# Kernel optimization log

Hardware: AMD Instinct MI355X
Metric: run time of the kernel (lower is better)

## Reference

```python
import jax, jax.numpy as jnp
import numpy as np

N_NODES = 50000
N_EDGES = 800000
D_FEAT = 128
D_EDGE = 64
N_HEADS = 4
OUT_DIM = 32
HID = N_HEADS * OUT_DIM  # 128


def segment_softmax(logits, seg, num_segments):
    # jraph.segment_softmax: subtract per-segment max, exp, normalize by per-segment sum
    seg_max = jax.ops.segment_max(logits, seg, num_segments=num_segments)
    e = jnp.exp(logits - seg_max[seg])
    denom = jax.ops.segment_sum(e, seg, num_segments=num_segments)
    return e / denom[seg]


def setup_inputs() -> dict:
    key = jax.random.key(0)
    ks = jax.random.split(key, 12)
    s = 1.0 / np.sqrt(D_FEAT)
    se = 1.0 / np.sqrt(D_EDGE)
    return {
        "nodes": jax.random.normal(ks[0], (N_NODES, D_FEAT), jnp.float32),
        "edges": jax.random.normal(ks[1], (N_EDGES, D_EDGE), jnp.float32),
        "senders": jax.random.randint(ks[2], (N_EDGES,), 0, N_NODES, jnp.int32),
        "receivers": jax.random.randint(ks[3], (N_EDGES,), 0, N_NODES, jnp.int32),
        "Wq": jax.random.normal(ks[4], (D_FEAT, HID), jnp.float32) * s,
        "bq": jnp.zeros((HID,), jnp.float32),
        "Wk": jax.random.normal(ks[5], (D_FEAT, HID), jnp.float32) * s,
        "bk": jnp.zeros((HID,), jnp.float32),
        "Wv": jax.random.normal(ks[6], (D_FEAT, HID), jnp.float32) * s,
        "bv": jnp.zeros((HID,), jnp.float32),
        "We": jax.random.normal(ks[7], (D_EDGE, HID), jnp.float32) * se,
        "Wu": jax.random.normal(ks[8], (D_FEAT, OUT_DIM), jnp.float32) * s,
        "bu": jnp.zeros((OUT_DIM,), jnp.float32),
    }


def reference(nodes, edges, senders, receivers, Wq, bq, Wk, bk, Wv, bv, We, Wu, bu):
    n_nodes = nodes.shape[0]
    send_feats = nodes[senders]    # [E, D]
    recv_feats = nodes[receivers]  # [E, D]

    q = (recv_feats @ Wq + bq).reshape(-1, N_HEADS, OUT_DIM)
    k = (send_feats @ Wk + bk).reshape(-1, N_HEADS, OUT_DIM)
    v = (send_feats @ Wv + bv).reshape(-1, N_HEADS, OUT_DIM)
    e = (edges @ We).reshape(-1, N_HEADS, OUT_DIM)

    attn = (q * k).sum(-1) / jnp.sqrt(jnp.asarray(OUT_DIM, q.dtype))  # [E, H]
    attn = segment_softmax(attn, receivers, n_nodes)                  # [E, H]

    msgs = (attn[:, :, None] * (v + e)).mean(axis=1)                  # [E, OUT_DIM]
    aggr = jax.ops.segment_sum(msgs, receivers, num_segments=n_nodes) # [N, OUT_DIM]

    feats = nodes @ Wu + bu
    return jax.nn.relu(feats + aggr)
```

## Files before the change

### kernel.cpp

```cpp
#include <hip/hip_runtime.h>
#include <math.h>

#define N_NODES 50000
#define N_EDGES 800000
#define D_FEAT 128
#define D_EDGE 64
#define HID 128
#define OUT_DIM 32

typedef unsigned short u16;
typedef short bf16x8 __attribute__((ext_vector_type(8)));
typedef float f32x4 __attribute__((ext_vector_type(4)));

__device__ __forceinline__ u16 f2bf(float x) {
    unsigned u = __float_as_uint(x);
    unsigned r = (u >> 16) & 1u;
    return (u16)((u + 0x7FFFu + r) >> 16);
}
__device__ __forceinline__ float bf2f(u16 s) { return __uint_as_float(((unsigned)s) << 16); }
__device__ __forceinline__ float bflo(unsigned u) { return __uint_as_float(u << 16); }
__device__ __forceinline__ float bfhi(unsigned u) { return __uint_as_float(u & 0xFFFF0000u); }

__global__ void zero_i32(int* __restrict__ p, int n) {
    int i = blockIdx.x * 256 + threadIdx.x;
    if (i < n) p[i] = 0;
}

__global__ void prep_weights(const float* __restrict__ Wq, const float* __restrict__ Wk,
                             const float* __restrict__ Wv, const float* __restrict__ We,
                             const float* __restrict__ Wu,
                             u16* __restrict__ WT_all, u16* __restrict__ WeTg) {
    int id = blockIdx.x * 256 + threadIdx.x;
    if (id < 49152) {
        int m = id >> 14, rem = id & 16383;
        int c = rem >> 7, k = rem & 127;
        const float* W = (m == 0) ? Wq : (m == 1) ? Wk : Wv;
        WT_all[id] = f2bf(W[k * HID + c]);
    } else if (id < 57344) {
        int j = id - 49152;
        int c = j >> 6, k = j & 63;
        WeTg[j] = f2bf(We[k * HID + c]);
    } else {
        int j = id - 57344;
        int c = j >> 7, k = j & 127;
        WT_all[49152 + j] = f2bf(Wu[k * OUT_DIM + c]);
    }
}

__global__ __launch_bounds__(256) void node_qkv_v3(
    const float* __restrict__ nodes, const u16* __restrict__ WT_all,
    const float* __restrict__ bq, const float* __restrict__ bk, const float* __restrict__ bv,
    const float* __restrict__ bu,
    u16* __restrict__ Q, u16* __restrict__ Kk, u16* __restrict__ Vp,
    float* __restrict__ baseout)
{
    __shared__ __align__(16) u16 Alds[4][32 * 136];

    const int tid = threadIdx.x;
    const int wave = tid >> 6, lane = tid & 63;
    const int quad = lane >> 4, l15 = lane & 15;
    const int rowbase = blockIdx.x * 128 + wave * 32;

    u16* As = &Alds[wave][0];
    #pragma unroll
    for (int it = 0; it < 16; ++it) {
        int idx = lane + it * 64;
        int row = idx >> 5, k4 = (idx & 31) * 4;
        float4 v = make_float4(0.f, 0.f, 0.f, 0.f);
        if (rowbase + row < N_NODES)
            v = *(const float4*)&nodes[(size_t)(rowbase + row) * D_FEAT + k4];
        ushort4 b;
        b.x = f2bf(v.x); b.y = f2bf(v.y); b.z = f2bf(v.z); b.w = f2bf(v.w);
        *(ushort4*)&As[row * 136 + k4] = b;
    }

    bf16x8 afr[2][4];
    #pragma unroll
    for (int rt = 0; rt < 2; ++rt)
        #pragma unroll
        for (int ks = 0; ks < 4; ++ks)
            afr[rt][ks] = *(const bf16x8*)&As[(rt * 16 + l15) * 136 + ks * 32 + quad * 8];

    #pragma unroll
    for (int m = 0; m < 3; ++m) {
        const u16* WT = WT_all + (size_t)m * 16384;
        const float* bvec = (m == 0) ? bq : (m == 1) ? bk : bv;
        u16* C = (m == 0) ? Q : (m == 1) ? Kk : Vp;

        f32x4 acc[2][8];
        #pragma unroll
        for (int rt = 0; rt < 2; ++rt)
            #pragma unroll
            for (int ct = 0; ct < 8; ++ct)
                acc[rt][ct] = (f32x4){0.f, 0.f, 0.f, 0.f};

        #pragma unroll
        for (int ks = 0; ks < 4; ++ks) {
            #pragma unroll
            for (int ct = 0; ct < 8; ++ct) {
                bf16x8 b = *(const bf16x8*)&WT[(ct * 16 + l15) * 128 + ks * 32 + quad * 8];
                acc[0][ct] = __builtin_amdgcn_mfma_f32_16x16x32_bf16(afr[0][ks], b, acc[0][ct], 0, 0, 0);
                acc[1][ct] = __builtin_amdgcn_mfma_f32_16x16x32_bf16(afr[1][ks], b, acc[1][ct], 0, 0, 0);
            }
        }

        #pragma unroll
        for (int ct = 0; ct < 8; ++ct) {
            int cbase = ct * 16 + l15;
            float bias = bvec[cbase];
            int oidx = (m == 2) ? ((cbase & 31) * 4 + (cbase >> 5)) : cbase;
            #pragma unroll
            for (int rt = 0; rt < 2; ++rt)
                #pragma unroll
                for (int r = 0; r < 4; ++r) {
                    int n = rowbase + rt * 16 + quad * 4 + r;
                    if (n < N_NODES)
                        C[(size_t)n * HID + oidx] = f2bf(acc[rt][ct][r] + bias);
                }
        }
    }

    {
        const u16* WuT = WT_all + 49152;
        f32x4 accu[2][2];
        #pragma unroll
        for (int rt = 0; rt < 2; ++rt)
            #pragma unroll
            for (int ct = 0; ct < 2; ++ct)
                accu[rt][ct] = (f32x4){0.f, 0.f, 0.f, 0.f};
        #pragma unroll
        for (int ks = 0; ks < 4; ++ks) {
            #pragma unroll
            for (int ct = 0; ct < 2; ++ct) {
                bf16x8 b = *(const bf16x8*)&WuT[(ct * 16 + l15) * 128 + ks * 32 + quad * 8];
                accu[0][ct] = __builtin_amdgcn_mfma_f32_16x16x32_bf16(afr[0][ks], b, accu[0][ct], 0, 0, 0);
                accu[1][ct] = __builtin_amdgcn_mfma_f32_16x16x32_bf16(afr[1][ks], b, accu[1][ct], 0, 0, 0);
            }
        }
        #pragma unroll
        for (int ct = 0; ct < 2; ++ct) {
            int cbase = ct * 16 + l15;
            float bias = bu[cbase];
            #pragma unroll
            for (int rt = 0; rt < 2; ++rt)
                #pragma unroll
                for (int r = 0; r < 4; ++r) {
                    int n = rowbase + rt * 16 + quad * 4 + r;
                    if (n < N_NODES)
                        baseout[(size_t)n * OUT_DIM + cbase] = accu[rt][ct][r] + bias;
                }
        }
    }
}

__global__ void hist_kernel(const int* __restrict__ receivers, int* __restrict__ count) {
    int e = blockIdx.x * 256 + threadIdx.x;
    atomicAdd(&count[receivers[e]], 1);
}

__global__ __launch_bounds__(256) void scan1(const int* __restrict__ count,
                                             int* __restrict__ incl, int* __restrict__ bsum) {
    __shared__ int sh[256];
    int gid = blockIdx.x * 256 + threadIdx.x;
    int v = (gid < N_NODES) ? count[gid] : 0;
    sh[threadIdx.x] = v; __syncthreads();
    #pragma unroll
    for (int off = 1; off < 256; off <<= 1) {
        int t = (threadIdx.x >= off) ? sh[threadIdx.x - off] : 0;
        __syncthreads();
        sh[threadIdx.x] += t;
        __syncthreads();
    }
    if (gid < N_NODES) incl[gid] = sh[threadIdx.x];
    if (threadIdx.x == 255) bsum[blockIdx.x] = sh[255];
}

__global__ __launch_bounds__(256) void scan2(const int* __restrict__ bsum,
                                             int* __restrict__ boff, int nblocks) {
    __shared__ int sh[256];
    int v = (threadIdx.x < nblocks) ? bsum[threadIdx.x] : 0;
    sh[threadIdx.x] = v; __syncthreads();
    #pragma unroll
    for (int off = 1; off < 256; off <<= 1) {
        int t = (threadIdx.x >= off) ? sh[threadIdx.x - off] : 0;
        __syncthreads();
        sh[threadIdx.x] += t;
        __syncthreads();
    }
    boff[threadIdx.x] = sh[threadIdx.x] - v;
}

__global__ __launch_bounds__(256) void scan3(const int* __restrict__ incl,
                                             const int* __restrict__ count,
                                             const int* __restrict__ boff,
                                             int* __restrict__ startp, int* __restrict__ cursor) {
    int gid = blockIdx.x * 256 + threadIdx.x;
    if (gid < N_NODES) {
        int ex = incl[gid] - count[gid] + boff[blockIdx.x];
        startp[gid] = ex;
        cursor[gid] = ex;
    }
    if (gid == 0) startp[N_NODES] = N_EDGES;
}

__global__ void scatter_v3(const int* __restrict__ senders, const int* __restrict__ receivers,
                           int* __restrict__ cursor, int* __restrict__ sorted,
                           int* __restrict__ ssend, int* __restrict__ srecv) {
    int e = blockIdx.x * 256 + threadIdx.x;
    int r = receivers[e];
    int s = senders[e];
    int pos = atomicAdd(&cursor[r], 1);
    sorted[pos] = e;
    ssend[pos] = s;
    srecv[pos] = r;
}

__global__ __launch_bounds__(256) void edge_logits_v3(
    const u16* __restrict__ Q, const u16* __restrict__ K,
    const int* __restrict__ ssend, const int* __restrict__ srecv,
    float* __restrict__ wbuf)
{
    int id = blockIdx.x * 256 + threadIdx.x;
    int i = id >> 1, half = id & 1;
    int s = ssend[i], r = srecv[i];
    const uint4* qp = (const uint4*)&Q[(size_t)r * HID + half * 64];
    const uint4* kp = (const uint4*)&K[(size_t)s * HID + half * 64];
    float a0 = 0.f, a1 = 0.f;
    #pragma unroll
    for (int j = 0; j < 4; ++j) {
        uint4 a = qp[j], b = kp[j];
        a0 += bflo(a.x) * bflo(b.x) + bfhi(a.x) * bfhi(b.x);
        a0 += bflo(a.y) * bflo(b.y) + bfhi(a.y) * bfhi(b.y);
        a0 += bflo(a.z) * bflo(b.z) + bfhi(a.z) * bfhi(b.z);
        a0 += bflo(a.w) * bflo(b.w) + bfhi(a.w) * bfhi(b.w);
    }
    #pragma unroll
    for (int j = 4; j < 8; ++j) {
        uint4 a = qp[j], b = kp[j];
        a1 += bflo(a.x) * bflo(b.x) + bfhi(a.x) * bfhi(b.x);
        a1 += bflo(a.y) * bflo(b.y) + bfhi(a.y) * bfhi(b.y);
        a1 += bflo(a.z) * bflo(b.z) + bfhi(a.z) * bfhi(b.z);
        a1 += bflo(a.w) * bflo(b.w) + bfhi(a.w) * bfhi(b.w);
    }
    const float sc = 0.17677669529663687f;
    float2 o = make_float2(expf(a0 * sc), expf(a1 * sc));
    *(float2*)&wbuf[(size_t)i * 4 + half * 2] = o;
}

__global__ __launch_bounds__(256) void denom_norm3(
    const int* __restrict__ startp, const int* __restrict__ sorted,
    const float* __restrict__ wbuf, float* __restrict__ wnorm)
{
    int id = blockIdx.x * 256 + threadIdx.x;
    int n = id >> 2, j = id & 3;
    if (n >= N_NODES) return;
    int s = startp[n], e = startp[n + 1];
    float4 a = make_float4(0.f, 0.f, 0.f, 0.f);
    for (int i = s + j; i < e; i += 4) {
        float4 w = *(const float4*)&wbuf[(size_t)i * 4];
        a.x += w.x; a.y += w.y; a.z += w.z; a.w += w.w;
    }
    #pragma unroll
    for (int off = 1; off < 4; off <<= 1) {
        a.x += __shfl_xor(a.x, off);
        a.y += __shfl_xor(a.y, off);
        a.z += __shfl_xor(a.z, off);
        a.w += __shfl_xor(a.w, off);
    }
    float4 inv;
    inv.x = 0.25f / a.x; inv.y = 0.25f / a.y; inv.z = 0.25f / a.z; inv.w = 0.25f / a.w;
    for (int i = s + j; i < e; i += 4) {
        float4 w = *(const float4*)&wbuf[(size_t)i * 4];
        w.x *= inv.x; w.y *= inv.y; w.z *= inv.z; w.w *= inv.w;
        *(float4*)&wnorm[(size_t)sorted[i] * 4] = w;
    }
}

__global__ __launch_bounds__(256) void edge_messages_v9(
    const float* __restrict__ edges, const u16* __restrict__ WeTg,
    const u16* __restrict__ Vp, const float* __restrict__ wnorm,
    const int* __restrict__ senders, u16* __restrict__ msg)
{
    __shared__ __align__(16) u16 Ae[4][32 * 72];

    const int tid = threadIdx.x;
    const int wave = tid >> 6, lane = tid & 63;
    const int quad = lane >> 4, l15 = lane & 15;
    const int base = blockIdx.x * 128 + wave * 32;

    int snd8[8];
    float w8[8][4];
    #pragma unroll
    for (int idx = 0; idx < 8; ++idx) {
        int el = base + (idx >> 2) * 16 + quad * 4 + (idx & 3);
        snd8[idx] = senders[el];
        float4 w = *(const float4*)&wnorm[(size_t)el * 4];
        w8[idx][0] = w.x; w8[idx][1] = w.y; w8[idx][2] = w.z; w8[idx][3] = w.w;
    }

    u16* As = &Ae[wave][0];
    #pragma unroll
    for (int it = 0; it < 8; ++it) {
        int idx = lane + it * 64;
        int row = idx >> 4, k4 = (idx & 15) * 4;
        float4 v = *(const float4*)&edges[(size_t)(base + row) * D_EDGE + k4];
        ushort4 b;
        b.x = f2bf(v.x); b.y = f2bf(v.y); b.z = f2bf(v.z); b.w = f2bf(v.w);
        *(ushort4*)&As[row * 72 + k4] = b;
    }

    bf16x8 afr[2][2];
    #pragma unroll
    for (int rt = 0; rt < 2; ++rt)
        #pragma unroll
        for (int ks = 0; ks < 2; ++ks)
            afr[rt][ks] = *(const bf16x8*)&As[(rt * 16 + l15) * 72 + ks * 32 + quad * 8];

    #pragma unroll
    for (int p = 0; p < 2; ++p) {
        const int d = p * 16 + l15;
        ushort4 vp8[8];
        #pragma unroll
        for (int idx = 0; idx < 8; ++idx)
            vp8[idx] = *(const ushort4*)&Vp[(size_t)snd8[idx] * HID + d * 4];

        f32x4 acc[2][4];
        #pragma unroll
        for (int rt = 0; rt < 2; ++rt)
            #pragma unroll
            for (int c = 0; c < 4; ++c)
                acc[rt][c] = (f32x4){0.f, 0.f, 0.f, 0.f};

        #pragma unroll
        for (int ks = 0; ks < 2; ++ks) {
            #pragma unroll
            for (int c = 0; c < 4; ++c) {
                bf16x8 b = *(const bf16x8*)&WeTg[((2 * c + p) * 16 + l15) * 64 + ks * 32 + quad * 8];
                acc[0][c] = __builtin_amdgcn_mfma_f32_16x16x32_bf16(afr[0][ks], b, acc[0][c], 0, 0, 0);
                acc[1][c] = __builtin_amdgcn_mfma_f32_16x16x32_bf16(afr[1][ks], b, acc[1][c], 0, 0, 0);
            }
        }

        #pragma unroll
        for (int idx = 0; idx < 8; ++idx) {
            int rt = idx >> 2, r = idx & 3;
            int el = base + rt * 16 + quad * 4 + r;
            float out = w8[idx][0] * (acc[rt][0][r] + bf2f(vp8[idx].x))
                      + w8[idx][1] * (acc[rt][1][r] + bf2f(vp8[idx].y))
                      + w8[idx][2] * (acc[rt][2][r] + bf2f(vp8[idx].z))
                      + w8[idx][3] * (acc[rt][3][r] + bf2f(vp8[idx].w));
            msg[(size_t)el * OUT_DIM + d] = f2bf(out);
        }
    }
}

__global__ __launch_bounds__(256) void aggregate4(
    const u16* __restrict__ msg, const float* __restrict__ baseout,
    const int* __restrict__ sorted, const int* __restrict__ startp,
    float* __restrict__ out)
{
    int id = blockIdx.x * 256 + threadIdx.x;
    int n = id >> 5, d = id & 31;
    float acc = baseout[id];
    int s = startp[n], e = startp[n + 1];
    for (int i = s; i < e; ++i) {
        int el = sorted[i];
        acc += bf2f(msg[(size_t)el * OUT_DIM + d]);
    }
    out[id] = fmaxf(acc, 0.f);
}

extern "C" void kernel_launch(void* const* d_in, const int* in_sizes, int n_in,
                              void* d_out, int out_size, void* d_ws, size_t ws_size,
                              hipStream_t stream) {
    const float* nodes     = (const float*)d_in[0];
    const float* edges     = (const float*)d_in[1];
    const int*   senders   = (const int*)d_in[2];
    const int*   receivers = (const int*)d_in[3];
    const float* Wq = (const float*)d_in[4];
    const float* bq = (const float*)d_in[5];
    const float* Wk = (const float*)d_in[6];
    const float* bk = (const float*)d_in[7];
    const float* Wv = (const float*)d_in[8];
    const float* bv = (const float*)d_in[9];
    const float* We = (const float*)d_in[10];
    const float* Wu = (const float*)d_in[11];
    const float* bu = (const float*)d_in[12];
    float* out = (float*)d_out;

    char* p = (char*)d_ws;
    u16* Qb    = (u16*)p; p += (size_t)N_NODES * HID * 2;
    u16* Kb    = (u16*)p; p += (size_t)N_NODES * HID * 2;
    u16* Vperm = (u16*)p; p += (size_t)N_NODES * HID * 2;
    u16* WT_all= (u16*)p; p += (size_t)(3 * HID * HID + OUT_DIM * HID) * 2;
    u16* WeTg  = (u16*)p; p += (size_t)HID * D_EDGE * 2;
    float* wbuf  = (float*)p; p += (size_t)N_EDGES * 4 * 4;
    float* wnorm = (float*)p; p += (size_t)N_EDGES * 4 * 4;
    u16* msg   = (u16*)p; p += (size_t)N_EDGES * OUT_DIM * 2;
    float* baseout = (float*)p; p += (size_t)N_NODES * OUT_DIM * 4;
    int* count  = (int*)p; p += (size_t)N_NODES * 4;
    int* incl   = (int*)p; p += (size_t)N_NODES * 4;
    int* startp = (int*)p; p += (size_t)(N_NODES + 4) * 4;
    int* cursor = (int*)p; p += (size_t)N_NODES * 4;
    int* sorted = (int*)p; p += (size_t)N_EDGES * 4;
    int* ssend  = (int*)p; p += (size_t)N_EDGES * 4;
    int* srecv  = (int*)p; p += (size_t)N_EDGES * 4;
    int* bsum   = (int*)p; p += 256 * 4;
    int* boff   = (int*)p; p += 256 * 4;

    const int SCAN_BLOCKS = (N_NODES + 255) / 256;

    hipLaunchKernelGGL(zero_i32, dim3(SCAN_BLOCKS), dim3(256), 0, stream, count, N_NODES);
    hipLaunchKernelGGL(hist_kernel, dim3(N_EDGES / 256), dim3(256), 0, stream,
                       receivers, count);
    hipLaunchKernelGGL(scan1, dim3(SCAN_BLOCKS), dim3(256), 0, stream, count, incl, bsum);
    hipLaunchKernelGGL(scan2, dim3(1), dim3(256), 0, stream, bsum, boff, SCAN_BLOCKS);
    hipLaunchKernelGGL(scan3, dim3(SCAN_BLOCKS), dim3(256), 0, stream,
                       incl, count, boff, startp, cursor);
    hipLaunchKernelGGL(scatter_v3, dim3(N_EDGES / 256), dim3(256), 0, stream,
                       senders, receivers, cursor, sorted, ssend, srecv);
    hipLaunchKernelGGL(prep_weights, dim3(61440 / 256), dim3(256), 0, stream,
                       Wq, Wk, Wv, We, Wu, WT_all, WeTg);
    hipLaunchKernelGGL(node_qkv_v3, dim3((N_NODES + 127) / 128), dim3(256), 0, stream,
                       nodes, WT_all, bq, bk, bv, bu, Qb, Kb, Vperm, baseout);
    hipLaunchKernelGGL(edge_logits_v3, dim3(N_EDGES * 2 / 256), dim3(256), 0, stream,
                       Qb, Kb, ssend, srecv, wbuf);
    hipLaunchKernelGGL(denom_norm3, dim3((N_NODES * 4 + 255) / 256), dim3(256), 0, stream,
                       startp, sorted, wbuf, wnorm);
    hipLaunchKernelGGL(edge_messages_v9, dim3(N_EDGES / 128), dim3(256), 0, stream,
                       edges, WeTg, Vperm, wnorm, senders, msg);
    hipLaunchKernelGGL(aggregate4, dim3(N_NODES * OUT_DIM / 256), dim3(256), 0, stream,
                       msg, baseout, sorted, startp, out);
}
```

Measured before the change: 621.9 us.

## Fold softmax denominator into logits kernel via atomics, drop denom pass

Removes the separate per-node denominator/normalize kernel. The logits kernel now accumulates exp sums into a per-node denominator buffer with float atomics. The messages kernel applies the normalization on the fly using a fast reciprocal. The scatter no longer writes sorted sender/receiver copies, so logits read them indirectly through the sorted index. The denominator buffer is zeroed together with the count array. This trades a kernel launch and two edge-sized buffers for atomic contention and extra indirect gathers, and atomic summation order makes the result nondeterministic.

Result: slower. 738.9 us (+18.8%).

```diff
diff --git a/kernel.cpp b/kernel.cpp
--- a/kernel.cpp
+++ b/kernel.cpp
@@ -203,26 +203,24 @@
     if (gid == 0) startp[N_NODES] = N_EDGES;
 }
 
-__global__ void scatter_v3(const int* __restrict__ senders, const int* __restrict__ receivers,
-                           int* __restrict__ cursor, int* __restrict__ sorted,
-                           int* __restrict__ ssend, int* __restrict__ srecv) {
+__global__ void scatter_v4(const int* __restrict__ receivers,
+                           int* __restrict__ cursor, int* __restrict__ sorted) {
     int e = blockIdx.x * 256 + threadIdx.x;
     int r = receivers[e];
-    int s = senders[e];
     int pos = atomicAdd(&cursor[r], 1);
     sorted[pos] = e;
-    ssend[pos] = s;
-    srecv[pos] = r;
-}
-
-__global__ __launch_bounds__(256) void edge_logits_v3(
+}
+
+__global__ __launch_bounds__(256) void edge_logits_v5(
     const u16* __restrict__ Q, const u16* __restrict__ K,
-    const int* __restrict__ ssend, const int* __restrict__ srecv,
-    float* __restrict__ wbuf)
+    const int* __restrict__ sorted, const int* __restrict__ senders,
+    const int* __restrict__ receivers,
+    float* __restrict__ wexp, float* __restrict__ denomv)
 {
     int id = blockIdx.x * 256 + threadIdx.x;
     int i = id >> 1, half = id & 1;
-    int s = ssend[i], r = srecv[i];
+    int e = sorted[i];
+    int s = senders[e], r = receivers[e];
     const uint4* qp = (const uint4*)&Q[(size_t)r * HID + half * 64];
     const uint4* kp = (const uint4*)&K[(size_t)s * HID + half * 64];
     float a0 = 0.f, a1 = 0.f;
@@ -244,42 +242,16 @@
     }
     const float sc = 0.17677669529663687f;
     float2 o = make_float2(expf(a0 * sc), expf(a1 * sc));
-    *(float2*)&wbuf[(size_t)i * 4 + half * 2] = o;
-}
-
-__global__ __launch_bounds__(256) void denom_norm3(
-    const int* __restrict__ startp, const int* __restrict__ sorted,
-    const float* __restrict__ wbuf, float* __restrict__ wnorm)
-{
-    int id = blockIdx.x * 256 + threadIdx.x;
-    int n = id >> 2, j = id & 3;
-    if (n >= N_NODES) return;
-    int s = startp[n], e = startp[n + 1];
-    float4 a = make_float4(0.f, 0.f, 0.f, 0.f);
-    for (int i = s + j; i < e; i += 4) {
-        float4 w = *(const float4*)&wbuf[(size_t)i * 4];
-        a.x += w.x; a.y += w.y; a.z += w.z; a.w += w.w;
-    }
-    #pragma unroll
-    for (int off = 1; off < 4; off <<= 1) {
-        a.x += __shfl_xor(a.x, off);
-        a.y += __shfl_xor(a.y, off);
-        a.z += __shfl_xor(a.z, off);
-        a.w += __shfl_xor(a.w, off);
-    }
-    float4 inv;
-    inv.x = 0.25f / a.x; inv.y = 0.25f / a.y; inv.z = 0.25f / a.z; inv.w = 0.25f / a.w;
-    for (int i = s + j; i < e; i += 4) {
-        float4 w = *(const float4*)&wbuf[(size_t)i * 4];
-        w.x *= inv.x; w.y *= inv.y; w.z *= inv.z; w.w *= inv.w;
-        *(float4*)&wnorm[(size_t)sorted[i] * 4] = w;
-    }
-}
-
-__global__ __launch_bounds__(256) void edge_messages_v9(
+    *(float2*)&wexp[(size_t)e * 4 + half * 2] = o;
+    atomicAdd(&denomv[(size_t)r * 4 + half * 2], o.x);
+    atomicAdd(&denomv[(size_t)r * 4 + half * 2 + 1], o.y);
+}
+
+__global__ __launch_bounds__(256, 4) void edge_messages_v10(
     const float* __restrict__ edges, const u16* __restrict__ WeTg,
-    const u16* __restrict__ Vp, const float* __restrict__ wnorm,
-    const int* __restrict__ senders, u16* __restrict__ msg)
+    const u16* __restrict__ Vp, const float* __restrict__ wexp,
+    const float* __restrict__ denomv, const int* __restrict__ senders,
+    const int* __restrict__ receivers, u16* __restrict__ msg)
 {
     __shared__ __align__(16) u16 Ae[4][32 * 72];
 
@@ -294,8 +266,13 @@
     for (int idx = 0; idx < 8; ++idx) {
         int el = base + (idx >> 2) * 16 + quad * 4 + (idx & 3);
         snd8[idx] = senders[el];
-        float4 w = *(const float4*)&wnorm[(size_t)el * 4];
-        w8[idx][0] = w.x; w8[idx][1] = w.y; w8[idx][2] = w.z; w8[idx][3] = w.w;
+        int r = receivers[el];
+        float4 we = *(const float4*)&wexp[(size_t)el * 4];
+        float4 dn = *(const float4*)&denomv[(size_t)r * 4];
+        w8[idx][0] = we.x * 0.25f * __builtin_amdgcn_rcpf(dn.x);
+        w8[idx][1] = we.y * 0.25f * __builtin_amdgcn_rcpf(dn.y);
+        w8[idx][2] = we.z * 0.25f * __builtin_amdgcn_rcpf(dn.z);
+        w8[idx][3] = we.w * 0.25f * __builtin_amdgcn_rcpf(dn.w);
     }
 
     u16* As = &Ae[wave][0];
@@ -314,7 +291,7 @@
     for (int rt = 0; rt < 2; ++rt)
         #pragma unroll
         for (int ks = 0; ks < 2; ++ks)
-            afr[rt][ks] = *(const bf16x8*)&As[(rt * 16 + l15) * 72 + ks * 32 + quad * 8];
+            afr[rt][ks] = *(const bf16x8*)&Ae[wave][(rt * 16 + l15) * 72 + ks * 32 + quad * 8];
 
     #pragma unroll
     for (int p = 0; p < 2; ++p) {
@@ -394,41 +371,39 @@
     u16* Vperm = (u16*)p; p += (size_t)N_NODES * HID * 2;
     u16* WT_all= (u16*)p; p += (size_t)(3 * HID * HID + OUT_DIM * HID) * 2;
     u16* WeTg  = (u16*)p; p += (size_t)HID * D_EDGE * 2;
-    float* wbuf  = (float*)p; p += (size_t)N_EDGES * 4 * 4;
-    float* wnorm = (float*)p; p += (size_t)N_EDGES * 4 * 4;
+    float* wexp = (float*)p; p += (size_t)N_EDGES * 4 * 4;
     u16* msg   = (u16*)p; p += (size_t)N_EDGES * OUT_DIM * 2;
     float* baseout = (float*)p; p += (size_t)N_NODES * OUT_DIM * 4;
     int* count  = (int*)p; p += (size_t)N_NODES * 4;
+    float* denomv = (float*)p; p += (size_t)N_NODES * 4 * 4;
     int* incl   = (int*)p; p += (size_t)N_NODES * 4;
     int* startp = (int*)p; p += (size_t)(N_NODES + 4) * 4;
     int* cursor = (int*)p; p += (size_t)N_NODES * 4;
     int* sorted = (int*)p; p += (size_t)N_EDGES * 4;
-    int* ssend  = (int*)p; p += (size_t)N_EDGES * 4;
-    int* srecv  = (int*)p; p += (size_t)N_EDGES * 4;
     int* bsum   = (int*)p; p += 256 * 4;
     int* boff   = (int*)p; p += 256 * 4;
 
     const int SCAN_BLOCKS = (N_NODES + 255) / 256;
-
-    hipLaunchKernelGGL(zero_i32, dim3(SCAN_BLOCKS), dim3(256), 0, stream, count, N_NODES);
+    const int ZERO_N = N_NODES + N_NODES * 4;
+
+    hipLaunchKernelGGL(zero_i32, dim3((ZERO_N + 255) / 256), dim3(256), 0, stream,
+                       count, ZERO_N);
     hipLaunchKernelGGL(hist_kernel, dim3(N_EDGES / 256), dim3(256), 0, stream,
                        receivers, count);
     hipLaunchKernelGGL(scan1, dim3(SCAN_BLOCKS), dim3(256), 0, stream, count, incl, bsum);
     hipLaunchKernelGGL(scan2, dim3(1), dim3(256), 0, stream, bsum, boff, SCAN_BLOCKS);
     hipLaunchKernelGGL(scan3, dim3(SCAN_BLOCKS), dim3(256), 0, stream,
                        incl, count, boff, startp, cursor);
-    hipLaunchKernelGGL(scatter_v3, dim3(N_EDGES / 256), dim3(256), 0, stream,
-                       senders, receivers, cursor, sorted, ssend, srecv);
+    hipLaunchKernelGGL(scatter_v4, dim3(N_EDGES / 256), dim3(256), 0, stream,
+                       receivers, cursor, sorted);
     hipLaunchKernelGGL(prep_weights, dim3(61440 / 256), dim3(256), 0, stream,
                        Wq, Wk, Wv, We, Wu, WT_all, WeTg);
     hipLaunchKernelGGL(node_qkv_v3, dim3((N_NODES + 127) / 128), dim3(256), 0, stream,
                        nodes, WT_all, bq, bk, bv, bu, Qb, Kb, Vperm, baseout);
-    hipLaunchKernelGGL(edge_logits_v3, dim3(N_EDGES * 2 / 256), dim3(256), 0, stream,
-                       Qb, Kb, ssend, srecv, wbuf);
-    hipLaunchKernelGGL(denom_norm3, dim3((N_NODES * 4 + 255) / 256), dim3(256), 0, stream,
-                       startp, sorted, wbuf, wnorm);
-    hipLaunchKernelGGL(edge_messages_v9, dim3(N_EDGES / 128), dim3(256), 0, stream,
-                       edges, WeTg, Vperm, wnorm, senders, msg);
+    hipLaunchKernelGGL(edge_logits_v5, dim3(N_EDGES * 2 / 256), dim3(256), 0, stream,
+                       Qb, Kb, sorted, senders, receivers, wexp, denomv);
+    hipLaunchKernelGGL(edge_messages_v10, dim3(N_EDGES / 128), dim3(256), 0, stream,
+                       edges, WeTg, Vperm, wexp, denomv, senders, receivers, msg);
     hipLaunchKernelGGL(aggregate4, dim3(N_NODES * OUT_DIM / 256), dim3(256), 0, stream,
                        msg, baseout, sorted, startp, out);
 }
```

## Fuse edge logits and softmax normalization into one wave-per-node kernel

Applied to the files above, without the earlier changes.

Replaces the per-edge logit kernel and the per-node denominator/normalize kernel with a single kernel in which one wavefront handles one receiver node. The node's Q row is loaded once into registers, exp logits for up to 96 edges stay in registers, and only higher-degree nodes spill to a scratch buffer. This removes the wbuf round trip, the srecv array and its writes in the scatter, and one kernel launch. In exchange, waves on low-degree nodes sit partly idle, and the per-chunk shuffle reductions add work.

Result: faster. 604.7 us (-2.8%).

```diff
diff --git a/kernel.cpp b/kernel.cpp
--- a/kernel.cpp
+++ b/kernel.cpp
@@ -20,6 +20,15 @@
 __device__ __forceinline__ float bf2f(u16 s) { return __uint_as_float(((unsigned)s) << 16); }
 __device__ __forceinline__ float bflo(unsigned u) { return __uint_as_float(u << 16); }
 __device__ __forceinline__ float bfhi(unsigned u) { return __uint_as_float(u & 0xFFFF0000u); }
+
+__device__ __forceinline__ float dot16(uint4 a, uint4 b) {
+    float s = 0.f;
+    s += bflo(a.x) * bflo(b.x) + bfhi(a.x) * bfhi(b.x);
+    s += bflo(a.y) * bflo(b.y) + bfhi(a.y) * bfhi(b.y);
+    s += bflo(a.z) * bflo(b.z) + bfhi(a.z) * bfhi(b.z);
+    s += bflo(a.w) * bflo(b.w) + bfhi(a.w) * bfhi(b.w);
+    return s;
+}
 
 __global__ void zero_i32(int* __restrict__ p, int n) {
     int i = blockIdx.x * 256 + threadIdx.x;
@@ -203,76 +212,97 @@
     if (gid == 0) startp[N_NODES] = N_EDGES;
 }
 
-__global__ void scatter_v3(const int* __restrict__ senders, const int* __restrict__ receivers,
+__global__ void scatter_v5(const int* __restrict__ senders, const int* __restrict__ receivers,
                            int* __restrict__ cursor, int* __restrict__ sorted,
-                           int* __restrict__ ssend, int* __restrict__ srecv) {
+                           int* __restrict__ ssend) {
     int e = blockIdx.x * 256 + threadIdx.x;
     int r = receivers[e];
     int s = senders[e];
     int pos = atomicAdd(&cursor[r], 1);
     sorted[pos] = e;
     ssend[pos] = s;
-    srecv[pos] = r;
-}
-
-__global__ __launch_bounds__(256) void edge_logits_v3(
+}
+
+__global__ __launch_bounds__(256) void node_softmax(
     const u16* __restrict__ Q, const u16* __restrict__ K,
-    const int* __restrict__ ssend, const int* __restrict__ srecv,
-    float* __restrict__ wbuf)
+    const int* __restrict__ startp, const int* __restrict__ sorted,
+    const int* __restrict__ ssend, float* __restrict__ wspill,
+    float* __restrict__ wnorm)
 {
-    int id = blockIdx.x * 256 + threadIdx.x;
-    int i = id >> 1, half = id & 1;
-    int s = ssend[i], r = srecv[i];
-    const uint4* qp = (const uint4*)&Q[(size_t)r * HID + half * 64];
-    const uint4* kp = (const uint4*)&K[(size_t)s * HID + half * 64];
-    float a0 = 0.f, a1 = 0.f;
-    #pragma unroll
-    for (int j = 0; j < 4; ++j) {
-        uint4 a = qp[j], b = kp[j];
-        a0 += bflo(a.x) * bflo(b.x) + bfhi(a.x) * bfhi(b.x);
-        a0 += bflo(a.y) * bflo(b.y) + bfhi(a.y) * bfhi(b.y);
-        a0 += bflo(a.z) * bflo(b.z) + bfhi(a.z) * bfhi(b.z);
-        a0 += bflo(a.w) * bflo(b.w) + bfhi(a.w) * bfhi(b.w);
-    }
-    #pragma unroll
-    for (int j = 4; j < 8; ++j) {
-        uint4 a = qp[j], b = kp[j];
-        a1 += bflo(a.x) * bflo(b.x) + bfhi(a.x) * bfhi(b.x);
-        a1 += bflo(a.y) * bflo(b.y) + bfhi(a.y) * bfhi(b.y);
-        a1 += bflo(a.z) * bflo(b.z) + bfhi(a.z) * bfhi(b.z);
-        a1 += bflo(a.w) * bflo(b.w) + bfhi(a.w) * bfhi(b.w);
-    }
+    const int wid = (blockIdx.x * 256 + threadIdx.x) >> 6;
+    const int lane = threadIdx.x & 63;
+    const int h = lane & 3, el = lane >> 2;
+    const int s0 = startp[wid];
+    const int deg = startp[wid + 1] - s0;
+    if (deg == 0) return;
+    const int nc = (deg + 15) >> 4;
     const float sc = 0.17677669529663687f;
-    float2 o = make_float2(expf(a0 * sc), expf(a1 * sc));
-    *(float2*)&wbuf[(size_t)i * 4 + half * 2] = o;
-}
-
-__global__ __launch_bounds__(256) void denom_norm3(
-    const int* __restrict__ startp, const int* __restrict__ sorted,
-    const float* __restrict__ wbuf, float* __restrict__ wnorm)
-{
-    int id = blockIdx.x * 256 + threadIdx.x;
-    int n = id >> 2, j = id & 3;
-    if (n >= N_NODES) return;
-    int s = startp[n], e = startp[n + 1];
-    float4 a = make_float4(0.f, 0.f, 0.f, 0.f);
-    for (int i = s + j; i < e; i += 4) {
-        float4 w = *(const float4*)&wbuf[(size_t)i * 4];
-        a.x += w.x; a.y += w.y; a.z += w.z; a.w += w.w;
-    }
-    #pragma unroll
-    for (int off = 1; off < 4; off <<= 1) {
-        a.x += __shfl_xor(a.x, off);
-        a.y += __shfl_xor(a.y, off);
-        a.z += __shfl_xor(a.z, off);
-        a.w += __shfl_xor(a.w, off);
-    }
-    float4 inv;
-    inv.x = 0.25f / a.x; inv.y = 0.25f / a.y; inv.z = 0.25f / a.z; inv.w = 0.25f / a.w;
-    for (int i = s + j; i < e; i += 4) {
-        float4 w = *(const float4*)&wbuf[(size_t)i * 4];
-        w.x *= inv.x; w.y *= inv.y; w.z *= inv.z; w.w *= inv.w;
-        *(float4*)&wnorm[(size_t)sorted[i] * 4] = w;
+
+    const uint4* qp = (const uint4*)&Q[(size_t)wid * HID + h * 32];
+    const uint4 q0 = qp[0], q1 = qp[1], q2 = qp[2], q3 = qp[3];
+
+    float expv0 = 0.f, expv1 = 0.f, expv2 = 0.f, expv3 = 0.f, expv4 = 0.f, expv5 = 0.f;
+    float dtot = 0.f;
+
+    #pragma unroll
+    for (int c = 0; c < 6; ++c) {
+        if (c >= nc) break;
+        int sl = c * 16 + el;
+        float w = 0.f;
+        if (sl < deg) {
+            int s = ssend[s0 + sl];
+            const uint4* kp = (const uint4*)&K[(size_t)s * HID + h * 32];
+            float a = dot16(q0, kp[0]) + dot16(q1, kp[1])
+                    + dot16(q2, kp[2]) + dot16(q3, kp[3]);
+            w = expf(a * sc);
+        }
+        if (c == 0) expv0 = w; else if (c == 1) expv1 = w; else if (c == 2) expv2 = w;
+        else if (c == 3) expv3 = w; else if (c == 4) expv4 = w; else expv5 = w;
+        float t = w;
+        t += __shfl_xor(t, 4); t += __shfl_xor(t, 8);
+        t += __shfl_xor(t, 16); t += __shfl_xor(t, 32);
+        dtot += t;
+    }
+    for (int c = 6; c < nc; ++c) {
+        int sl = c * 16 + el;
+        float w = 0.f;
+        if (sl < deg) {
+            int s = ssend[s0 + sl];
+            const uint4* kp = (const uint4*)&K[(size_t)s * HID + h * 32];
+            float a = dot16(q0, kp[0]) + dot16(q1, kp[1])
+                    + dot16(q2, kp[2]) + dot16(q3, kp[3]);
+            w = expf(a * sc);
+            wspill[(size_t)(s0 + sl) * 4 + h] = w;
+        }
+        float t = w;
+        t += __shfl_xor(t, 4); t += __shfl_xor(t, 8);
+        t += __shfl_xor(t, 16); t += __shfl_xor(t, 32);
+        dtot += t;
+    }
+
+    const float inv = 0.25f / dtot;
+
+    #pragma unroll
+    for (int c = 0; c < 6; ++c) {
+        if (c >= nc) break;
+        int sl = c * 16 + el;
+        if (sl < deg) {
+            float w = (c == 0) ? expv0 : (c == 1) ? expv1 : (c == 2) ? expv2
+                    : (c == 3) ? expv3 : (c == 4) ? expv4 : expv5;
+            int e = sorted[s0 + sl];
+            wnorm[(size_t)e * 4 + h] = w * inv;
+        }
+    }
+    if (nc > 6) {
+        asm volatile("s_waitcnt vmcnt(0)" ::: "memory");
+        for (int c = 6; c < nc; ++c) {
+            int sl = c * 16 + el;
+            if (sl < deg) {
+                float w = wspill[(size_t)(s0 + sl) * 4 + h];
+                int e = sorted[s0 + sl];
+                wnorm[(size_t)e * 4 + h] = w * inv;
+            }
+        }
     }
 }
 
@@ -394,8 +424,8 @@
     u16* Vperm = (u16*)p; p += (size_t)N_NODES * HID * 2;
     u16* WT_all= (u16*)p; p += (size_t)(3 * HID * HID + OUT_DIM * HID) * 2;
     u16* WeTg  = (u16*)p; p += (size_t)HID * D_EDGE * 2;
-    float* wbuf  = (float*)p; p += (size_t)N_EDGES * 4 * 4;
-    float* wnorm = (float*)p; p += (size_t)N_EDGES * 4 * 4;
+    float* wspill = (float*)p; p += (size_t)N_EDGES * 4 * 4;
+    float* wnorm  = (float*)p; p += (size_t)N_EDGES * 4 * 4;
     u16* msg   = (u16*)p; p += (size_t)N_EDGES * OUT_DIM * 2;
     float* baseout = (float*)p; p += (size_t)N_NODES * OUT_DIM * 4;
     int* count  = (int*)p; p += (size_t)N_NODES * 4;
@@ -404,7 +434,6 @@
     int* cursor = (int*)p; p += (size_t)N_NODES * 4;
     int* sorted = (int*)p; p += (size_t)N_EDGES * 4;
     int* ssend  = (int*)p; p += (size_t)N_EDGES * 4;
-    int* srecv  = (int*)p; p += (size_t)N_EDGES * 4;
     int* bsum   = (int*)p; p += 256 * 4;
     int* boff   = (int*)p; p += 256 * 4;
 
@@ -417,16 +446,14 @@
     hipLaunchKernelGGL(scan2, dim3(1), dim3(256), 0, stream, bsum, boff, SCAN_BLOCKS);
     hipLaunchKernelGGL(scan3, dim3(SCAN_BLOCKS), dim3(256), 0, stream,
                        incl, count, boff, startp, cursor);
-    hipLaunchKernelGGL(scatter_v3, dim3(N_EDGES / 256), dim3(256), 0, stream,
-                       senders, receivers, cursor, sorted, ssend, srecv);
+    hipLaunchKernelGGL(scatter_v5, dim3(N_EDGES / 256), dim3(256), 0, stream,
+                       senders, receivers, cursor, sorted, ssend);
     hipLaunchKernelGGL(prep_weights, dim3(61440 / 256), dim3(256), 0, stream,
                        Wq, Wk, Wv, We, Wu, WT_all, WeTg);
     hipLaunchKernelGGL(node_qkv_v3, dim3((N_NODES + 127) / 128), dim3(256), 0, stream,
                        nodes, WT_all, bq, bk, bv, bu, Qb, Kb, Vperm, baseout);
-    hipLaunchKernelGGL(edge_logits_v3, dim3(N_EDGES * 2 / 256), dim3(256), 0, stream,
-                       Qb, Kb, ssend, srecv, wbuf);
-    hipLaunchKernelGGL(denom_norm3, dim3((N_NODES * 4 + 255) / 256), dim3(256), 0, stream,
-                       startp, sorted, wbuf, wnorm);
+    hipLaunchKernelGGL(node_softmax, dim3(N_NODES / 4), dim3(256), 0, stream,
+                       Qb, Kb, startp, sorted, ssend, wspill, wnorm);
     hipLaunchKernelGGL(edge_messages_v9, dim3(N_EDGES / 128), dim3(256), 0, stream,
                        edges, WeTg, Vperm, wnorm, senders, msg);
     hipLaunchKernelGGL(aggregate4, dim3(N_NODES * OUT_DIM / 256), dim3(256), 0, stream,
```
